# Performance work log

Hardware: AMD Instinct MI355X
Metric: run time of the kernel (lower is better)

## Reference

```python
import jax, jax.numpy as jnp
import numpy as np

# pywt db4 decomposition filters (dec_lo, dec_hi), length 8
DB4_DEC_LO = np.array([-0.010597401784997278, 0.032883011666982945,
                       0.030841381835986965, -0.18703481171888114,
                       -0.02798376941698385, 0.6308807679295904,
                       0.7148465705525415, 0.23037781330885523], dtype=np.float32)
DB4_DEC_HI = np.array([-0.23037781330885523, 0.7148465705525415,
                       -0.6308807679295904, -0.02798376941698385,
                       0.18703481171888114, 0.030841381835986965,
                       -0.032883011666982945, -0.010597401784997278], dtype=np.float32)
LEVEL = 3


def setup_inputs() -> dict:
    key = jax.random.key(0)
    x = jax.random.normal(key, (64, 32, 4096), dtype=jnp.float32)  # (B, N, T)
    return {"x": x,
            "dec_lo": jnp.asarray(DB4_DEC_LO),
            "dec_hi": jnp.asarray(DB4_DEC_HI)}


def _swt(x, dec_lo, dec_hi, level=LEVEL):
    """Stationary (a trous) wavelet transform, matching ptwt.swt semantics."""
    B, N, T = x.shape
    filt_len = dec_lo.shape[0]
    # ptwt flips the filters so conv1d (correlation) performs true convolution
    filt = jnp.stack([dec_lo[::-1], dec_hi[::-1]], axis=0)[:, None, :]  # (2, 1, L)
    res_lo = x.reshape(B * N, 1, T)
    details = []
    for lvl in range(level):
        dil = 2 ** lvl
        padl = dil * (filt_len // 2 - 1)
        padr = dil * (filt_len // 2)
        padded = jnp.pad(res_lo, ((0, 0), (0, 0), (padl, padr)), mode="wrap")  # circular
        res = jax.lax.conv_general_dilated(
            padded, filt, window_strides=(1,), padding="VALID",
            rhs_dilation=(dil,), dimension_numbers=("NCH", "OIH", "NCH"))  # (BN, 2, T)
        res_lo = res[:, 0:1, :]
        details.append(res[:, 1, :])
    # ptwt ordering: [cA_level, cD_level, ..., cD_1]
    coeffs = [res_lo[:, 0, :]] + details[::-1]
    stacked = jnp.stack(coeffs, axis=1)  # (B*N, level+1, T)
    return stacked.reshape(B, N, level + 1, T).transpose(0, 1, 3, 2)  # (B, N, T, level+1)


def reference(x, dec_lo, dec_hi):
    return _swt(x, dec_lo, dec_hi)
```

## Files before the change

### kernel.cpp

```cpp
#include <hip/hip_runtime.h>

#define TLEN 4096
#define NT 256
#define PER 16
#define SH 12
#define RH 16
#define BUFLEN (SH + TLEN + RH)

typedef float f32x4 __attribute__((ext_vector_type(4)));
typedef float f32x2 __attribute__((ext_vector_type(2)));

__device__ __forceinline__ f32x4 ldv4(const float* p) {
    return *reinterpret_cast<const f32x4*>(p);
}

__global__ __launch_bounds__(NT, 4) void swt_db4_l3_kernel(
    const float* __restrict__ x,
    const float* __restrict__ lo_g,
    const float* __restrict__ hi_g,
    float* __restrict__ out)
{
    __shared__ float bufA[BUFLEN];
    __shared__ float bufB[BUFLEN];

    const int row = blockIdx.x;
    const int tid = threadIdx.x;

    f32x2 c[8];
#pragma unroll
    for (int j = 0; j < 8; ++j) { c[j].x = lo_g[j]; c[j].y = hi_g[j]; }

    const float* xr = x + (size_t)row * TLEN;

#pragma unroll
    for (int k = 0; k < 4; ++k) {
        int idx = (tid + k * NT) * 4;
        f32x4 v = ldv4(xr + idx);
        *reinterpret_cast<f32x4*>(&bufA[SH + idx]) = v;
        if (k == 0 && tid < 4)
            *reinterpret_cast<f32x4*>(&bufA[SH + TLEN + idx]) = v;
        if (k == 3 && idx >= TLEN - SH)
            *reinterpret_cast<f32x4*>(&bufA[idx - (TLEN - SH)]) = v;
    }
    __syncthreads();

    float D1[PER], D2[PER];

#pragma unroll
    for (int k = 0; k < PER; ++k) {
        int t = tid + k * NT;
        const float* s = &bufA[t + SH];
        f32x2 acc; acc.x = 0.f; acc.y = 0.f;
#pragma unroll
        for (int j = 0; j < 8; ++j) {
            float v = s[(4 - j)];
            f32x2 vv; vv.x = v; vv.y = v;
            acc = __builtin_elementwise_fma(c[j], vv, acc);
        }
        bufB[t + SH] = acc.x;
        if (k == 0 && tid < RH)           bufB[t + SH + TLEN] = acc.x;
        if (k == PER - 1 && t >= TLEN - SH) bufB[t + SH - TLEN] = acc.x;
        D1[k] = acc.y;
    }
    __syncthreads();

#pragma unroll
    for (int k = 0; k < PER; ++k) {
        int t = tid + k * NT;
        const float* s = &bufB[t + SH];
        f32x2 acc; acc.x = 0.f; acc.y = 0.f;
#pragma unroll
        for (int j = 0; j < 8; ++j) {
            float v = s[(4 - j) * 2];
            f32x2 vv; vv.x = v; vv.y = v;
            acc = __builtin_elementwise_fma(c[j], vv, acc);
        }
        bufA[t + SH] = acc.x;
        if (k == 0 && tid < RH)           bufA[t + SH + TLEN] = acc.x;
        if (k == PER - 1 && t >= TLEN - SH) bufA[t + SH - TLEN] = acc.x;
        D2[k] = acc.y;
    }
    __syncthreads();

    f32x4* outr = reinterpret_cast<f32x4*>(out + (size_t)row * TLEN * 4);
#pragma unroll
    for (int k = 0; k < PER; ++k) {
        int t = tid + k * NT;
        const float* s = &bufA[t + SH];
        f32x2 acc; acc.x = 0.f; acc.y = 0.f;
#pragma unroll
        for (int j = 0; j < 8; ++j) {
            float v = s[(4 - j) * 4];
            f32x2 vv; vv.x = v; vv.y = v;
            acc = __builtin_elementwise_fma(c[j], vv, acc);
        }
        f32x4 o;
        o.x = acc.x;
        o.y = acc.y;
        o.z = D2[k];
        o.w = D1[k];
        outr[t] = o;
    }
}

extern "C" void kernel_launch(void* const* d_in, const int* in_sizes, int n_in,
                              void* d_out, int out_size, void* d_ws, size_t ws_size,
                              hipStream_t stream) {
    const float* x  = (const float*)d_in[0];
    const float* lo = (const float*)d_in[1];
    const float* hi = (const float*)d_in[2];
    float* out = (float*)d_out;

    const int rows = 64 * 32;
    swt_db4_l3_kernel<<<dim3(rows), dim3(NT), 0, stream>>>(x, lo, hi, out);
}
```

Measured before the change: 32.77 us.

## Split each row into per-wave segments with halos to remove block barriers

After: 36.50 us. 11.4% more time.

```diff
diff --git a/kernel.cpp b/kernel.cpp
--- a/kernel.cpp
+++ b/kernel.cpp
@@ -2,10 +2,10 @@
 
 #define TLEN 4096
 #define NT 256
-#define PER 16
-#define SH 12
-#define RH 16
-#define BUFLEN (SH + TLEN + RH)
+#define SEG 1024
+#define OFF 24
+#define RHW 32
+#define BUFW 1088
 
 typedef float f32x4 __attribute__((ext_vector_type(4)));
 typedef float f32x2 __attribute__((ext_vector_type(2)));
@@ -20,11 +20,15 @@
     const float* __restrict__ hi_g,
     float* __restrict__ out)
 {
-    __shared__ float bufA[BUFLEN];
-    __shared__ float bufB[BUFLEN];
+    __shared__ float lds[4 * 2 * BUFW];
 
-    const int row = blockIdx.x;
-    const int tid = threadIdx.x;
+    const int wave = threadIdx.x >> 6;
+    const int lane = threadIdx.x & 63;
+    const int row  = blockIdx.x;
+    const int seg  = wave * SEG;
+
+    float* bufX = &lds[wave * 2 * BUFW];
+    float* bufY = bufX + BUFW;
 
     f32x2 c[8];
 #pragma unroll
@@ -34,59 +38,57 @@
 
 #pragma unroll
     for (int k = 0; k < 4; ++k) {
-        int idx = (tid + k * NT) * 4;
-        f32x4 v = ldv4(xr + idx);
-        *reinterpret_cast<f32x4*>(&bufA[SH + idx]) = v;
-        if (k == 0 && tid < 4)
-            *reinterpret_cast<f32x4*>(&bufA[SH + TLEN + idx]) = v;
-        if (k == 3 && idx >= TLEN - SH)
-            *reinterpret_cast<f32x4*>(&bufA[idx - (TLEN - SH)]) = v;
+        int q = lane + k * 64;
+        *reinterpret_cast<f32x4*>(&bufX[OFF + 4 * q]) = ldv4(xr + seg + 4 * q);
     }
-    __syncthreads();
+    if (lane < OFF)
+        bufX[lane] = xr[(seg - OFF + lane) & (TLEN - 1)];
+    if (lane < RHW)
+        bufX[OFF + SEG + lane] = xr[(seg + SEG + lane) & (TLEN - 1)];
 
-    float D1[PER], D2[PER];
+    float D1e[18], D2e[18];
 
 #pragma unroll
-    for (int k = 0; k < PER; ++k) {
-        int t = tid + k * NT;
-        const float* s = &bufA[t + SH];
+    for (int k = 0; k < 18; ++k) {
+        int u = -64 + lane + 64 * k;
         f32x2 acc; acc.x = 0.f; acc.y = 0.f;
+        bool act = (k > 0 && k < 17) || (u >= -18 && u < 1048);
+        if (act) {
+            const float* s = &bufX[OFF + u];
 #pragma unroll
-        for (int j = 0; j < 8; ++j) {
-            float v = s[(4 - j)];
-            f32x2 vv; vv.x = v; vv.y = v;
-            acc = __builtin_elementwise_fma(c[j], vv, acc);
+            for (int j = 0; j < 8; ++j) {
+                float v = s[4 - j];
+                f32x2 vv; vv.x = v; vv.y = v;
+                acc = __builtin_elementwise_fma(c[j], vv, acc);
+            }
+            bufY[OFF + u] = acc.x;
         }
-        bufB[t + SH] = acc.x;
-        if (k == 0 && tid < RH)           bufB[t + SH + TLEN] = acc.x;
-        if (k == PER - 1 && t >= TLEN - SH) bufB[t + SH - TLEN] = acc.x;
-        D1[k] = acc.y;
+        D1e[k] = acc.y;
     }
-    __syncthreads();
 
 #pragma unroll
-    for (int k = 0; k < PER; ++k) {
-        int t = tid + k * NT;
-        const float* s = &bufB[t + SH];
+    for (int k = 0; k < 18; ++k) {
+        int u = -64 + lane + 64 * k;
         f32x2 acc; acc.x = 0.f; acc.y = 0.f;
+        bool act = (k > 0 && k < 17) || (u >= -12 && u < 1040);
+        if (act) {
+            const float* s = &bufY[OFF + u];
 #pragma unroll
-        for (int j = 0; j < 8; ++j) {
-            float v = s[(4 - j) * 2];
-            f32x2 vv; vv.x = v; vv.y = v;
-            acc = __builtin_elementwise_fma(c[j], vv, acc);
+            for (int j = 0; j < 8; ++j) {
+                float v = s[(4 - j) * 2];
+                f32x2 vv; vv.x = v; vv.y = v;
+                acc = __builtin_elementwise_fma(c[j], vv, acc);
+            }
+            bufX[OFF + u] = acc.x;
         }
-        bufA[t + SH] = acc.x;
-        if (k == 0 && tid < RH)           bufA[t + SH + TLEN] = acc.x;
-        if (k == PER - 1 && t >= TLEN - SH) bufA[t + SH - TLEN] = acc.x;
-        D2[k] = acc.y;
+        D2e[k] = acc.y;
     }
-    __syncthreads();
 
-    f32x4* outr = reinterpret_cast<f32x4*>(out + (size_t)row * TLEN * 4);
+    f32x4* outr = reinterpret_cast<f32x4*>(out + (size_t)row * TLEN * 4) + seg;
 #pragma unroll
-    for (int k = 0; k < PER; ++k) {
-        int t = tid + k * NT;
-        const float* s = &bufA[t + SH];
+    for (int k = 0; k < 16; ++k) {
+        int t = lane + 64 * k;
+        const float* s = &bufX[OFF + t];
         f32x2 acc; acc.x = 0.f; acc.y = 0.f;
 #pragma unroll
         for (int j = 0; j < 8; ++j) {
@@ -97,8 +99,8 @@
         f32x4 o;
         o.x = acc.x;
         o.y = acc.y;
-        o.z = D2[k];
-        o.w = D1[k];
+        o.z = D2e[k + 1];
+        o.w = D1e[k + 1];
         outr[t] = o;
     }
 }
```

## Split each row into two half-segments per block with halo recomputation

Applied to the files above, without the earlier changes.

New measurement: 32.43 us. About the same (-1.0%).

```diff
diff --git a/kernel.cpp b/kernel.cpp
--- a/kernel.cpp
+++ b/kernel.cpp
@@ -2,10 +2,10 @@
 
 #define TLEN 4096
 #define NT 256
-#define PER 16
-#define SH 12
-#define RH 16
-#define BUFLEN (SH + TLEN + RH)
+#define SEG 2048
+#define PER 8
+#define OFF 24
+#define BUFW 2112
 
 typedef float f32x4 __attribute__((ext_vector_type(4)));
 typedef float f32x2 __attribute__((ext_vector_type(2)));
@@ -14,16 +14,18 @@
     return *reinterpret_cast<const f32x4*>(p);
 }
 
-__global__ __launch_bounds__(NT, 4) void swt_db4_l3_kernel(
+__global__ __launch_bounds__(NT, 8) void swt_db4_l3_kernel(
     const float* __restrict__ x,
     const float* __restrict__ lo_g,
     const float* __restrict__ hi_g,
     float* __restrict__ out)
 {
-    __shared__ float bufA[BUFLEN];
-    __shared__ float bufB[BUFLEN];
+    __shared__ float bufX[BUFW];
+    __shared__ float bufY[BUFW];
 
-    const int row = blockIdx.x;
+    const int bid = blockIdx.x;
+    const int row = bid >> 1;
+    const int seg = (bid & 1) << 11;
     const int tid = threadIdx.x;
 
     f32x2 c[8];
@@ -33,14 +35,13 @@
     const float* xr = x + (size_t)row * TLEN;
 
 #pragma unroll
-    for (int k = 0; k < 4; ++k) {
+    for (int k = 0; k < 2; ++k) {
         int idx = (tid + k * NT) * 4;
-        f32x4 v = ldv4(xr + idx);
-        *reinterpret_cast<f32x4*>(&bufA[SH + idx]) = v;
-        if (k == 0 && tid < 4)
-            *reinterpret_cast<f32x4*>(&bufA[SH + TLEN + idx]) = v;
-        if (k == 3 && idx >= TLEN - SH)
-            *reinterpret_cast<f32x4*>(&bufA[idx - (TLEN - SH)]) = v;
+        *reinterpret_cast<f32x4*>(&bufX[OFF + idx]) = ldv4(xr + seg + idx);
+    }
+    if (tid < 49) {
+        int u = (tid < 21) ? (tid - 21) : (SEG + tid - 21);
+        bufX[OFF + u] = xr[(seg + u) & (TLEN - 1)];
     }
     __syncthreads();
 
@@ -49,25 +50,31 @@
 #pragma unroll
     for (int k = 0; k < PER; ++k) {
         int t = tid + k * NT;
-        const float* s = &bufA[t + SH];
+        const float* s = &bufX[OFF + t];
         f32x2 acc; acc.x = 0.f; acc.y = 0.f;
 #pragma unroll
         for (int j = 0; j < 8; ++j) {
-            float v = s[(4 - j)];
+            float v = s[4 - j];
             f32x2 vv; vv.x = v; vv.y = v;
             acc = __builtin_elementwise_fma(c[j], vv, acc);
         }
-        bufB[t + SH] = acc.x;
-        if (k == 0 && tid < RH)           bufB[t + SH + TLEN] = acc.x;
-        if (k == PER - 1 && t >= TLEN - SH) bufB[t + SH - TLEN] = acc.x;
+        bufY[OFF + t] = acc.x;
         D1[k] = acc.y;
+    }
+    if (tid < 42) {
+        int u = (tid < 18) ? (tid - 18) : (SEG + tid - 18);
+        const float* s = &bufX[OFF + u];
+        float a = 0.f;
+#pragma unroll
+        for (int j = 0; j < 8; ++j) a = fmaf(c[j].x, s[4 - j], a);
+        bufY[OFF + u] = a;
     }
     __syncthreads();
 
 #pragma unroll
     for (int k = 0; k < PER; ++k) {
         int t = tid + k * NT;
-        const float* s = &bufB[t + SH];
+        const float* s = &bufY[OFF + t];
         f32x2 acc; acc.x = 0.f; acc.y = 0.f;
 #pragma unroll
         for (int j = 0; j < 8; ++j) {
@@ -75,18 +82,24 @@
             f32x2 vv; vv.x = v; vv.y = v;
             acc = __builtin_elementwise_fma(c[j], vv, acc);
         }
-        bufA[t + SH] = acc.x;
-        if (k == 0 && tid < RH)           bufA[t + SH + TLEN] = acc.x;
-        if (k == PER - 1 && t >= TLEN - SH) bufA[t + SH - TLEN] = acc.x;
+        bufX[OFF + t] = acc.x;
         D2[k] = acc.y;
+    }
+    if (tid < 28) {
+        int u = (tid < 12) ? (tid - 12) : (SEG + tid - 12);
+        const float* s = &bufY[OFF + u];
+        float a = 0.f;
+#pragma unroll
+        for (int j = 0; j < 8; ++j) a = fmaf(c[j].x, s[(4 - j) * 2], a);
+        bufX[OFF + u] = a;
     }
     __syncthreads();
 
-    f32x4* outr = reinterpret_cast<f32x4*>(out + (size_t)row * TLEN * 4);
+    f32x4* outr = reinterpret_cast<f32x4*>(out + (size_t)row * TLEN * 4) + seg;
 #pragma unroll
     for (int k = 0; k < PER; ++k) {
         int t = tid + k * NT;
-        const float* s = &bufA[t + SH];
+        const float* s = &bufX[OFF + t];
         f32x2 acc; acc.x = 0.f; acc.y = 0.f;
 #pragma unroll
         for (int j = 0; j < 8; ++j) {
@@ -111,6 +124,6 @@
     const float* hi = (const float*)d_in[2];
     float* out = (float*)d_out;
 
-    const int rows = 64 * 32;
-    swt_db4_l3_kernel<<<dim3(rows), dim3(NT), 0, stream>>>(x, lo, hi, out);
+    const int nblocks = 64 * 32 * 2;
+    swt_db4_l3_kernel<<<dim3(nblocks), dim3(NT), 0, stream>>>(x, lo, hi, out);
 }
```
